# Performance work log

Measured on AMD Instinct MI355X. Metric: run time of the kernel, lower is better.

The kernel has to match this reference:

```python
import jax, jax.numpy as jnp
import numpy as np

H = 512  # hidden_dim

def _gru_dir(x, w_ih, w_hh, b_ih, b_hh, reverse):
    """One direction of one GRU layer. x: [B,T,D]. Returns (outputs [B,T,H], h_T [B,H])."""
    B = x.shape[0]
    # Precompute input-to-gate projections for all timesteps: [T,B,3H]
    xg = (jnp.einsum('btd,gd->btg', x, w_ih) + b_ih).transpose(1, 0, 2)
    if reverse:
        xg = jnp.flip(xg, axis=0)

    def step(h, xg_t):
        hg = h @ w_hh.T + b_hh                      # [B,3H]
        xr, xz, xn = jnp.split(xg_t, 3, axis=-1)
        hr, hz, hn = jnp.split(hg, 3, axis=-1)
        r = jax.nn.sigmoid(xr + hr)
        z = jax.nn.sigmoid(xz + hz)
        n = jnp.tanh(xn + r * hn)
        h_new = (1.0 - z) * n + z * h
        return h_new, h_new

    h0 = jnp.zeros((B, H), dtype=x.dtype)
    hT, hs = jax.lax.scan(step, h0, xg)             # hs: [T,B,H]
    if reverse:
        hs = jnp.flip(hs, axis=0)
    return hs.transpose(1, 0, 2), hT


def _bigru_layer(x, w_ih, w_hh, b_ih, b_hh):
    """Bidirectional layer; stacked weights have leading dim 2 = [fwd, bwd]."""
    out_f, hT_f = _gru_dir(x, w_ih[0], w_hh[0], b_ih[0], b_hh[0], reverse=False)
    out_b, hT_b = _gru_dir(x, w_ih[1], w_hh[1], b_ih[1], b_hh[1], reverse=True)
    return jnp.concatenate([out_f, out_b], axis=-1), hT_f, hT_b


def setup_inputs() -> dict:
    key = jax.random.key(0)
    ks = jax.random.split(key, 12)
    s = 1.0 / np.sqrt(H)
    inp = {
        'sentence': jax.random.randint(ks[0], (64, 512), 0, 50000),
        'emb':      jax.random.normal(ks[1], (50000, 256), jnp.float32) * 0.1,
        'w_ih_l0':  jax.random.normal(ks[2], (2, 3 * H, 256), jnp.float32) * s,
        'w_hh_l0':  jax.random.normal(ks[3], (2, 3 * H, H), jnp.float32) * s,
        'b_ih_l0':  jax.random.normal(ks[4], (2, 3 * H), jnp.float32) * s,
        'b_hh_l0':  jax.random.normal(ks[5], (2, 3 * H), jnp.float32) * s,
        'w_ih_l1':  jax.random.normal(ks[6], (2, 3 * H, 2 * H), jnp.float32) * s,
        'w_hh_l1':  jax.random.normal(ks[7], (2, 3 * H, H), jnp.float32) * s,
        'b_ih_l1':  jax.random.normal(ks[8], (2, 3 * H), jnp.float32) * s,
        'b_hh_l1':  jax.random.normal(ks[9], (2, 3 * H), jnp.float32) * s,
        'fc_w':     jax.random.normal(ks[10], (10, 2 * H), jnp.float32) * s,
        'fc_b':     jax.random.normal(ks[11], (10,), jnp.float32) * s,
    }
    return inp


def reference(sentence, emb, w_ih_l0, w_hh_l0, b_ih_l0, b_hh_l0,
              w_ih_l1, w_hh_l1, b_ih_l1, b_hh_l1, fc_w, fc_b):
    x = emb[sentence]                                # [B,T,E] embedding lookup
    x, _, _ = _bigru_layer(x, w_ih_l0, w_hh_l0, b_ih_l0, b_hh_l0)  # [B,T,2H]
    # dropout is inactive in eval mode
    _, hT_f, hT_b = _bigru_layer(x, w_ih_l1, w_hh_l1, b_ih_l1, b_hh_l1)
    hidden = jnp.concatenate([hT_f, hT_b], axis=1)   # [B,2H] = cat(h[-2], h[-1])
    return hidden @ fc_w.T + fc_b                    # [B,n_classes]
```

## Files before the change

### kernel.cpp

```cpp
#include <hip/hip_runtime.h>
#include <stdint.h>

#define H   512
#define B   64
#define T   512
#define E   256
#define G3  1536
#define CT  64
#define NBG 4
#define NUG 32

typedef short s16;
typedef unsigned short u16;
typedef unsigned int u32;
typedef __attribute__((ext_vector_type(8))) short   short8;
typedef __attribute__((ext_vector_type(4))) float   f32x4;
typedef __attribute__((ext_vector_type(4))) unsigned int u32x4;
typedef __attribute__((ext_vector_type(2))) unsigned int u32x2;
typedef __bf16 bf8_t __attribute__((ext_vector_type(8)));

__device__ __forceinline__ u16 f2b(float f) {
    union { float f; unsigned int i; } v; v.f = f;
    unsigned int r = v.i + 0x7FFF + ((v.i >> 16) & 1);
    return (u16)(r >> 16);
}
__device__ __forceinline__ float sigm(float x)  { return 1.f / (1.f + __expf(-x)); }
__device__ __forceinline__ float tanhs(float x) { return 1.f - 2.f / (1.f + __expf(2.f * x)); }

__global__ void k_cvt(const float* __restrict__ src, u16* __restrict__ dst, int n) {
    int i = blockIdx.x * 256 + threadIdx.x;
    int stride = gridDim.x * 256;
    for (; i < n; i += stride) dst[i] = f2b(src[i]);
}

__global__ void k_init(float* __restrict__ h32, u32* __restrict__ slots) {
    int i = blockIdx.x * 256 + threadIdx.x;
    slots[i] = 0;
    if (i < 65536) h32[i] = 0.f;
}

#define BM 128
#define BN 128
#define BK 32

__global__ __launch_bounds__(256)
void k_gemm_xg(const int* __restrict__ sent, const void* __restrict__ Abuf, int aIsF32,
               const u16* __restrict__ Wbf, const float* __restrict__ bih,
               float* __restrict__ xgT, int K, int c) {
    int d  = blockIdx.z;
    int t0 = d ? (T - (c + 1) * CT) : c * CT;
    const u16* Bw = Wbf + (long)d * G3 * K;
    const float* bias = bih + (long)d * G3;
    float* C = xgT + (long)d * (long)CT * G3 * B;

    __shared__ __align__(16) s16 lA[BM * BK];
    __shared__ __align__(16) s16 lB[BN * BK];

    int tid  = threadIdx.x;
    int lane = tid & 63;
    int wv   = tid >> 6;
    int wm   = wv >> 1, wn = wv & 1;
    int q    = lane >> 4, r16 = lane & 15;

    long m0 = (long)blockIdx.x * BM;
    long n0 = (long)blockIdx.y * BN;

    const float* rowAf[2];
    const s16*   rowAh[2];
    const u16*   rowB[2];
    #pragma unroll
    for (int i = 0; i < 2; i++) {
        int ch = tid + i * 256;
        int r  = ch >> 2, cc = (ch & 3) * 8;
        long m = m0 + r;
        int  bb_ = (int)(m & 63), tl = (int)(m >> 6);
        int  t  = t0 + tl;
        if (aIsF32) rowAf[i] = (const float*)Abuf + (long)sent[bb_ * T + t] * K + cc;
        else        rowAh[i] = (const s16*)Abuf + ((long)bb_ * T + t) * K + cc;
        rowB[i] = Bw + (n0 + r) * K + cc;
    }

    f32x4 acc[4][4];
    #pragma unroll
    for (int i = 0; i < 4; i++)
        #pragma unroll
        for (int j = 0; j < 4; j++) acc[i][j] = (f32x4){0.f, 0.f, 0.f, 0.f};

    for (long k0 = 0; k0 < K; k0 += BK) {
        #pragma unroll
        for (int i = 0; i < 2; i++) {
            if (aIsF32) {
                float4 v0 = *(const float4*)(rowAf[i] + k0);
                float4 v1 = *(const float4*)(rowAf[i] + k0 + 4);
                short8 pk;
                pk[0] = (s16)f2b(v0.x); pk[1] = (s16)f2b(v0.y);
                pk[2] = (s16)f2b(v0.z); pk[3] = (s16)f2b(v0.w);
                pk[4] = (s16)f2b(v1.x); pk[5] = (s16)f2b(v1.y);
                pk[6] = (s16)f2b(v1.z); pk[7] = (s16)f2b(v1.w);
                ((short8*)lA)[tid + i * 256] = pk;
            } else {
                ((short8*)lA)[tid + i * 256] = *(const short8*)(rowAh[i] + k0);
            }
            ((short8*)lB)[tid + i * 256] = *(const short8*)((const s16*)rowB[i] + k0);
        }
        __syncthreads();

        bf8_t af[4], bf[4];
        #pragma unroll
        for (int mt = 0; mt < 4; mt++)
            af[mt] = ((const bf8_t*)lA)[(wm * 64 + mt * 16 + r16) * 4 + q];
        #pragma unroll
        for (int nt = 0; nt < 4; nt++)
            bf[nt] = ((const bf8_t*)lB)[(wn * 64 + nt * 16 + r16) * 4 + q];
        #pragma unroll
        for (int mt = 0; mt < 4; mt++)
            #pragma unroll
            for (int nt = 0; nt < 4; nt++)
                acc[mt][nt] = __builtin_amdgcn_mfma_f32_16x16x32_bf16(
                                  bf[nt], af[mt], acc[mt][nt], 0, 0, 0);
        __syncthreads();
    }

    #pragma unroll
    for (int nt = 0; nt < 4; nt++) {
        f32x4 bv = *(const f32x4*)(bias + n0 + wn * 64 + nt * 16 + q * 4);
        #pragma unroll
        for (int mt = 0; mt < 4; mt++) {
            long m = m0 + wm * 64 + mt * 16 + r16;
            long tl = m >> 6, b = m & 63;
            #pragma unroll
            for (int rg = 0; rg < 4; rg++) {
                long n = n0 + wn * 64 + nt * 16 + q * 4 + rg;
                C[(tl * G3 + n) * B + b] = acc[mt][nt][rg] + bv[rg];
            }
        }
    }
}

__global__ __launch_bounds__(64, 1)
void k_chunk(const u16* __restrict__ Whhbf, const float* __restrict__ bhh,
             const float* __restrict__ xgT, float* __restrict__ h32,
             u32* __restrict__ slots, int c, u16* __restrict__ x1out, int writeX1) {
    int ug = blockIdx.x;
    int bg = blockIdx.y;
    int d  = blockIdx.z;
    int lane = threadIdx.x;
    int q = lane >> 4, cc = lane & 15;
    int u0 = ug * 16;
    int bgl = bg * 16 + cc;

    const u16* W    = Whhbf + (long)d * G3 * H;
    const float* bb = bhh + (long)d * G3;
    const float* xgf = xgT + (long)d * (long)CT * G3 * B;
    float* h32d = h32 + (long)d * B * H;
    char* slotbase = (char*)slots;

    bf8_t w[3][16];
    #pragma unroll
    for (int gate = 0; gate < 3; gate++)
        #pragma unroll
        for (int kc = 0; kc < 16; kc++)
            w[gate][kc] = *(const bf8_t*)(W + (long)(gate * H + u0 + cc) * H + kc * 32 + q * 8);

    f32x4 brv = *(const f32x4*)(bb + u0 + q * 4);
    f32x4 bzv = *(const f32x4*)(bb + H + u0 + q * 4);
    f32x4 bnv = *(const f32x4*)(bb + 2 * H + u0 + q * 4);

    f32x4 hp = *(const f32x4*)(h32d + (long)bgl * H + u0 + q * 4);

    int jw = ug * 4 + q;
    long off_wr = (long)((jw >> 3) * 2 + (jw & 1)) * 1024
                + (long)((jw >> 1) & 3) * 256 + cc * 16;

    int base = c * CT;

    for (int sl = 0; sl < CT; sl++) {
        int s    = base + sl;
        int tl   = d ? (CT - 1 - sl) : sl;
        int time = d ? (T - 1 - s) : s;
        int tgt  = s;
        u32 st1  = (u32)(s + 1);

        const float* xgb = xgf + ((long)tl * G3 + u0 + q * 4) * B + bgl;
        float xr[4], xz[4], xn[4];
        #pragma unroll
        for (int jj = 0; jj < 4; jj++) {
            xr[jj] = xgb[(long)jj * B];
            xz[jj] = xgb[(long)H * B + (long)jj * B];
            xn[jj] = xgb[(long)2 * H * B + (long)jj * B];
        }

        const char* domb = slotbase + (long)(((d * 2 + (s & 1)) * 4 + bg) * 32768);
        const char* pb  = domb + lane * 16;
        const char* qa0 = pb;
        const char* qa1 = pb + 4096;
        const char* qa2 = pb + 8192;
        const char* qa3 = pb + 12288;
        const char* qa4 = pb + 16384;
        const char* qa5 = pb + 20480;
        const char* qa6 = pb + 24576;
        const char* qa7 = pb + 28672;
        u32x4 p0,p1,p2,p3,p4,p5,p6,p7,p8,p9,p10,p11,p12,p13,p14,p15;
        u32x4 p16,p17,p18,p19,p20,p21,p22,p23,p24,p25,p26,p27,p28,p29,p30,p31;

        for (;;) {
            asm volatile(
                "global_load_dwordx4 %0,  %16, off sc0 sc1\n\t"
                "global_load_dwordx4 %1,  %16, off offset:1024 sc0 sc1\n\t"
                "global_load_dwordx4 %2,  %16, off offset:2048 sc0 sc1\n\t"
                "global_load_dwordx4 %3,  %16, off offset:3072 sc0 sc1\n\t"
                "global_load_dwordx4 %4,  %17, off sc0 sc1\n\t"
                "global_load_dwordx4 %5,  %17, off offset:1024 sc0 sc1\n\t"
                "global_load_dwordx4 %6,  %17, off offset:2048 sc0 sc1\n\t"
                "global_load_dwordx4 %7,  %17, off offset:3072 sc0 sc1\n\t"
                "global_load_dwordx4 %8,  %18, off sc0 sc1\n\t"
                "global_load_dwordx4 %9,  %18, off offset:1024 sc0 sc1\n\t"
                "global_load_dwordx4 %10, %18, off offset:2048 sc0 sc1\n\t"
                "global_load_dwordx4 %11, %18, off offset:3072 sc0 sc1\n\t"
                "global_load_dwordx4 %12, %19, off sc0 sc1\n\t"
                "global_load_dwordx4 %13, %19, off offset:1024 sc0 sc1\n\t"
                "global_load_dwordx4 %14, %19, off offset:2048 sc0 sc1\n\t"
                "global_load_dwordx4 %15, %19, off offset:3072 sc0 sc1"
                : "=&v"(p0),"=&v"(p1),"=&v"(p2),"=&v"(p3),
                  "=&v"(p4),"=&v"(p5),"=&v"(p6),"=&v"(p7),
                  "=&v"(p8),"=&v"(p9),"=&v"(p10),"=&v"(p11),
                  "=&v"(p12),"=&v"(p13),"=&v"(p14),"=&v"(p15)
                : "v"(qa0), "v"(qa1), "v"(qa2), "v"(qa3)
                : "memory");
            asm volatile(
                "global_load_dwordx4 %0,  %16, off sc0 sc1\n\t"
                "global_load_dwordx4 %1,  %16, off offset:1024 sc0 sc1\n\t"
                "global_load_dwordx4 %2,  %16, off offset:2048 sc0 sc1\n\t"
                "global_load_dwordx4 %3,  %16, off offset:3072 sc0 sc1\n\t"
                "global_load_dwordx4 %4,  %17, off sc0 sc1\n\t"
                "global_load_dwordx4 %5,  %17, off offset:1024 sc0 sc1\n\t"
                "global_load_dwordx4 %6,  %17, off offset:2048 sc0 sc1\n\t"
                "global_load_dwordx4 %7,  %17, off offset:3072 sc0 sc1\n\t"
                "global_load_dwordx4 %8,  %18, off sc0 sc1\n\t"
                "global_load_dwordx4 %9,  %18, off offset:1024 sc0 sc1\n\t"
                "global_load_dwordx4 %10, %18, off offset:2048 sc0 sc1\n\t"
                "global_load_dwordx4 %11, %18, off offset:3072 sc0 sc1\n\t"
                "global_load_dwordx4 %12, %19, off sc0 sc1\n\t"
                "global_load_dwordx4 %13, %19, off offset:1024 sc0 sc1\n\t"
                "global_load_dwordx4 %14, %19, off offset:2048 sc0 sc1\n\t"
                "global_load_dwordx4 %15, %19, off offset:3072 sc0 sc1\n\t"
                "s_waitcnt vmcnt(0)"
                : "=&v"(p16),"=&v"(p17),"=&v"(p18),"=&v"(p19),
                  "=&v"(p20),"=&v"(p21),"=&v"(p22),"=&v"(p23),
                  "=&v"(p24),"=&v"(p25),"=&v"(p26),"=&v"(p27),
                  "=&v"(p28),"=&v"(p29),"=&v"(p30),"=&v"(p31)
                : "v"(qa4), "v"(qa5), "v"(qa6), "v"(qa7)
                : "memory");
            __builtin_amdgcn_sched_barrier(0);
            int mn = min((int)p0[1], (int)p0[3]);
            #define MN2(x) mn = min(mn, min((int)x[1], (int)x[3]));
            MN2(p1)  MN2(p2)  MN2(p3)  MN2(p4)  MN2(p5)  MN2(p6)  MN2(p7)
            MN2(p8)  MN2(p9)  MN2(p10) MN2(p11) MN2(p12) MN2(p13) MN2(p14) MN2(p15)
            MN2(p16) MN2(p17) MN2(p18) MN2(p19) MN2(p20) MN2(p21) MN2(p22) MN2(p23)
            MN2(p24) MN2(p25) MN2(p26) MN2(p27) MN2(p28) MN2(p29) MN2(p30) MN2(p31)
            #undef MN2
            if (__all(mn >= tgt)) break;
        }

        f32x4 aR = (f32x4){0.f,0.f,0.f,0.f};
        f32x4 aZ = (f32x4){0.f,0.f,0.f,0.f};
        f32x4 aN = (f32x4){0.f,0.f,0.f,0.f};
        #define STEP_KC(kc, A_, B_) { \
            u32x4 fw = (u32x4){A_[0], A_[2], B_[0], B_[2]}; \
            bf8_t hb = __builtin_bit_cast(bf8_t, fw); \
            aR = __builtin_amdgcn_mfma_f32_16x16x32_bf16(w[0][kc], hb, aR, 0, 0, 0); \
            aZ = __builtin_amdgcn_mfma_f32_16x16x32_bf16(w[1][kc], hb, aZ, 0, 0, 0); \
            aN = __builtin_amdgcn_mfma_f32_16x16x32_bf16(w[2][kc], hb, aN, 0, 0, 0); }
        STEP_KC(0,  p0,  p1)  STEP_KC(1,  p2,  p3)  STEP_KC(2,  p4,  p5)  STEP_KC(3,  p6,  p7)
        STEP_KC(4,  p8,  p9)  STEP_KC(5,  p10, p11) STEP_KC(6,  p12, p13) STEP_KC(7,  p14, p15)
        STEP_KC(8,  p16, p17) STEP_KC(9,  p18, p19) STEP_KC(10, p20, p21) STEP_KC(11, p22, p23)
        STEP_KC(12, p24, p25) STEP_KC(13, p26, p27) STEP_KC(14, p28, p29) STEP_KC(15, p30, p31)
        #undef STEP_KC

        float hh[4];
        #pragma unroll
        for (int rg = 0; rg < 4; rg++) {
            float r = sigm(xr[rg] + aR[rg] + brv[rg]);
            float z = sigm(xz[rg] + aZ[rg] + bzv[rg]);
            float n = tanhs(xn[rg] + r * (aN[rg] + bnv[rg]));
            hh[rg] = (1.f - z) * n + z * hp[rg];
        }
        hp = (f32x4){hh[0], hh[1], hh[2], hh[3]};

        u32 w0 = (u32)f2b(hh[0]) | ((u32)f2b(hh[1]) << 16);
        u32 w1 = (u32)f2b(hh[2]) | ((u32)f2b(hh[3]) << 16);
        u32x4 sv = (u32x4){w0, st1, w1, st1};
        char* ps = slotbase + (long)(((d * 2 + ((s + 1) & 1)) * 4 + bg) * 32768) + off_wr;
        asm volatile("global_store_dwordx4 %0, %1, off sc0 sc1"
                     :: "v"(ps), "v"(sv) : "memory");

        if (writeX1) {
            u32x2 xv = (u32x2){w0, w1};
            *(u32x2*)(x1out + ((long)bgl * T + time) * 1024 + d * H + u0 + q * 4) = xv;
        }
    }

    *(f32x4*)(h32d + (long)bgl * H + u0 + q * 4) = hp;
}

__global__ __launch_bounds__(256)
void k_fc(const float* __restrict__ h32, const float* __restrict__ fcw,
          const float* __restrict__ fcb, float* __restrict__ out) {
    int b   = blockIdx.x;
    int tid = threadIdx.x;
    float p[10];
    #pragma unroll
    for (int o = 0; o < 10; o++) p[o] = 0.f;
    for (int k = tid; k < 1024; k += 256) {
        int dd = k >> 9, kk = k & 511;
        float hv = h32[(long)dd * B * H + (long)b * H + kk];
        #pragma unroll
        for (int o = 0; o < 10; o++) p[o] += hv * fcw[o * 1024 + k];
    }
    __shared__ float red[10][256];
    #pragma unroll
    for (int o = 0; o < 10; o++) red[o][tid] = p[o];
    __syncthreads();
    for (int off = 128; off > 0; off >>= 1) {
        if (tid < off)
            #pragma unroll
            for (int o = 0; o < 10; o++) red[o][tid] += red[o][tid + off];
        __syncthreads();
    }
    if (tid < 10) out[b * 10 + tid] = red[tid][0] + fcb[tid];
}

extern "C" void kernel_launch(void* const* d_in, const int* in_sizes, int n_in,
                              void* d_out, int out_size, void* d_ws, size_t ws_size,
                              hipStream_t stream) {
    const int*   sent = (const int*)d_in[0];
    const float* emb  = (const float*)d_in[1];
    const float* wih0 = (const float*)d_in[2];
    const float* whh0 = (const float*)d_in[3];
    const float* bih0 = (const float*)d_in[4];
    const float* bhh0 = (const float*)d_in[5];
    const float* wih1 = (const float*)d_in[6];
    const float* whh1 = (const float*)d_in[7];
    const float* bih1 = (const float*)d_in[8];
    const float* bhh1 = (const float*)d_in[9];
    const float* fcw  = (const float*)d_in[10];
    const float* fcb  = (const float*)d_in[11];
    float* outp = (float*)d_out;

    char*  ws  = (char*)d_ws;
    float* xg  = (float*)(ws);
    u16*   x1  = (u16*)(ws + 50331648L);
    float* h32 = (float*)(ws + 50331648L + 67108864L);
    u32*   slt = (u32*)(ws + 50331648L + 67108864L + 262144L);
    u16*   wbf = (u16*)(ws + 50331648L + 67108864L + 262144L + 524288L);
    u16* wih0b = wbf;
    u16* wih1b = wbf + 786432L;
    u16* whh0b = wbf + 786432L + 3145728L;
    u16* whh1b = whh0b + 1572864L;

    k_cvt<<<512, 256, 0, stream>>>(wih0, wih0b, 786432);
    k_cvt<<<512, 256, 0, stream>>>(wih1, wih1b, 3145728);
    k_cvt<<<512, 256, 0, stream>>>(whh0, whh0b, 1572864);
    k_cvt<<<512, 256, 0, stream>>>(whh1, whh1b, 1572864);

    dim3 gg(32, 12, 2);
    dim3 gc(NUG, NBG, 2);

    k_init<<<512, 256, 0, stream>>>(h32, slt);
    for (int c = 0; c < T / CT; c++) {
        k_gemm_xg<<<gg, 256, 0, stream>>>(sent, emb, 1, wih0b, bih0, xg, E, c);
        k_chunk<<<gc, 64, 0, stream>>>(whh0b, bhh0, xg, h32, slt, c, x1, 1);
    }

    k_init<<<512, 256, 0, stream>>>(h32, slt);
    for (int c = 0; c < T / CT; c++) {
        k_gemm_xg<<<gg, 256, 0, stream>>>(sent, x1, 0, wih1b, bih1, xg, 2 * H, c);
        k_chunk<<<gc, 64, 0, stream>>>(whh1b, bhh1, xg, h32, slt, c, (u16*)nullptr, 0);
    }

    k_fc<<<B, 256, 0, stream>>>(h32, fcw, fcb, outp);
}
```

Before: 3.314 ms.

## Use XCD-local cache scope for slot polling with fallback, remap blocks per domain

```diff
diff --git a/kernel.cpp b/kernel.cpp
--- a/kernel.cpp
+++ b/kernel.cpp
@@ -137,13 +137,64 @@
     }
 }
 
+#define BULK(SC) \
+    asm volatile( \
+        "global_load_dwordx4 %0,  %16, off " SC "\n\t" \
+        "global_load_dwordx4 %1,  %16, off offset:1024 " SC "\n\t" \
+        "global_load_dwordx4 %2,  %16, off offset:2048 " SC "\n\t" \
+        "global_load_dwordx4 %3,  %16, off offset:3072 " SC "\n\t" \
+        "global_load_dwordx4 %4,  %17, off " SC "\n\t" \
+        "global_load_dwordx4 %5,  %17, off offset:1024 " SC "\n\t" \
+        "global_load_dwordx4 %6,  %17, off offset:2048 " SC "\n\t" \
+        "global_load_dwordx4 %7,  %17, off offset:3072 " SC "\n\t" \
+        "global_load_dwordx4 %8,  %18, off " SC "\n\t" \
+        "global_load_dwordx4 %9,  %18, off offset:1024 " SC "\n\t" \
+        "global_load_dwordx4 %10, %18, off offset:2048 " SC "\n\t" \
+        "global_load_dwordx4 %11, %18, off offset:3072 " SC "\n\t" \
+        "global_load_dwordx4 %12, %19, off " SC "\n\t" \
+        "global_load_dwordx4 %13, %19, off offset:1024 " SC "\n\t" \
+        "global_load_dwordx4 %14, %19, off offset:2048 " SC "\n\t" \
+        "global_load_dwordx4 %15, %19, off offset:3072 " SC \
+        : "=&v"(p0),"=&v"(p1),"=&v"(p2),"=&v"(p3), \
+          "=&v"(p4),"=&v"(p5),"=&v"(p6),"=&v"(p7), \
+          "=&v"(p8),"=&v"(p9),"=&v"(p10),"=&v"(p11), \
+          "=&v"(p12),"=&v"(p13),"=&v"(p14),"=&v"(p15) \
+        : "v"(qa0), "v"(qa1), "v"(qa2), "v"(qa3) \
+        : "memory"); \
+    asm volatile( \
+        "global_load_dwordx4 %0,  %16, off " SC "\n\t" \
+        "global_load_dwordx4 %1,  %16, off offset:1024 " SC "\n\t" \
+        "global_load_dwordx4 %2,  %16, off offset:2048 " SC "\n\t" \
+        "global_load_dwordx4 %3,  %16, off offset:3072 " SC "\n\t" \
+        "global_load_dwordx4 %4,  %17, off " SC "\n\t" \
+        "global_load_dwordx4 %5,  %17, off offset:1024 " SC "\n\t" \
+        "global_load_dwordx4 %6,  %17, off offset:2048 " SC "\n\t" \
+        "global_load_dwordx4 %7,  %17, off offset:3072 " SC "\n\t" \
+        "global_load_dwordx4 %8,  %18, off " SC "\n\t" \
+        "global_load_dwordx4 %9,  %18, off offset:1024 " SC "\n\t" \
+        "global_load_dwordx4 %10, %18, off offset:2048 " SC "\n\t" \
+        "global_load_dwordx4 %11, %18, off offset:3072 " SC "\n\t" \
+        "global_load_dwordx4 %12, %19, off " SC "\n\t" \
+        "global_load_dwordx4 %13, %19, off offset:1024 " SC "\n\t" \
+        "global_load_dwordx4 %14, %19, off offset:2048 " SC "\n\t" \
+        "global_load_dwordx4 %15, %19, off offset:3072 " SC "\n\t" \
+        "s_waitcnt vmcnt(0)" \
+        : "=&v"(p16),"=&v"(p17),"=&v"(p18),"=&v"(p19), \
+          "=&v"(p20),"=&v"(p21),"=&v"(p22),"=&v"(p23), \
+          "=&v"(p24),"=&v"(p25),"=&v"(p26),"=&v"(p27), \
+          "=&v"(p28),"=&v"(p29),"=&v"(p30),"=&v"(p31) \
+        : "v"(qa4), "v"(qa5), "v"(qa6), "v"(qa7) \
+        : "memory");
+
 __global__ __launch_bounds__(64, 1)
 void k_chunk(const u16* __restrict__ Whhbf, const float* __restrict__ bhh,
              const float* __restrict__ xgT, float* __restrict__ h32,
              u32* __restrict__ slots, int c, u16* __restrict__ x1out, int writeX1) {
-    int ug = blockIdx.x;
-    int bg = blockIdx.y;
-    int d  = blockIdx.z;
+    int bid = blockIdx.x;
+    int dom = bid & 7;
+    int ug  = bid >> 3;
+    int d   = dom >> 2;
+    int bg  = dom & 3;
     int lane = threadIdx.x;
     int q = lane >> 4, cc = lane & 15;
     int u0 = ug * 16;
@@ -173,6 +224,7 @@
                 + (long)((jw >> 1) & 3) * 256 + cc * 16;
 
     int base = c * CT;
+    bool fast = true;
 
     for (int sl = 0; sl < CT; sl++) {
         int s    = base + sl;
@@ -203,54 +255,10 @@
         u32x4 p0,p1,p2,p3,p4,p5,p6,p7,p8,p9,p10,p11,p12,p13,p14,p15;
         u32x4 p16,p17,p18,p19,p20,p21,p22,p23,p24,p25,p26,p27,p28,p29,p30,p31;
 
+        int fails = 0;
         for (;;) {
-            asm volatile(
-                "global_load_dwordx4 %0,  %16, off sc0 sc1\n\t"
-                "global_load_dwordx4 %1,  %16, off offset:1024 sc0 sc1\n\t"
-                "global_load_dwordx4 %2,  %16, off offset:2048 sc0 sc1\n\t"
-                "global_load_dwordx4 %3,  %16, off offset:3072 sc0 sc1\n\t"
-                "global_load_dwordx4 %4,  %17, off sc0 sc1\n\t"
-                "global_load_dwordx4 %5,  %17, off offset:1024 sc0 sc1\n\t"
-                "global_load_dwordx4 %6,  %17, off offset:2048 sc0 sc1\n\t"
-                "global_load_dwordx4 %7,  %17, off offset:3072 sc0 sc1\n\t"
-                "global_load_dwordx4 %8,  %18, off sc0 sc1\n\t"
-                "global_load_dwordx4 %9,  %18, off offset:1024 sc0 sc1\n\t"
-                "global_load_dwordx4 %10, %18, off offset:2048 sc0 sc1\n\t"
-                "global_load_dwordx4 %11, %18, off offset:3072 sc0 sc1\n\t"
-                "global_load_dwordx4 %12, %19, off sc0 sc1\n\t"
-                "global_load_dwordx4 %13, %19, off offset:1024 sc0 sc1\n\t"
-                "global_load_dwordx4 %14, %19, off offset:2048 sc0 sc1\n\t"
-                "global_load_dwordx4 %15, %19, off offset:3072 sc0 sc1"
-                : "=&v"(p0),"=&v"(p1),"=&v"(p2),"=&v"(p3),
-                  "=&v"(p4),"=&v"(p5),"=&v"(p6),"=&v"(p7),
-                  "=&v"(p8),"=&v"(p9),"=&v"(p10),"=&v"(p11),
-                  "=&v"(p12),"=&v"(p13),"=&v"(p14),"=&v"(p15)
-                : "v"(qa0), "v"(qa1), "v"(qa2), "v"(qa3)
-                : "memory");
-            asm volatile(
-                "global_load_dwordx4 %0,  %16, off sc0 sc1\n\t"
-                "global_load_dwordx4 %1,  %16, off offset:1024 sc0 sc1\n\t"
-                "global_load_dwordx4 %2,  %16, off offset:2048 sc0 sc1\n\t"
-                "global_load_dwordx4 %3,  %16, off offset:3072 sc0 sc1\n\t"
-                "global_load_dwordx4 %4,  %17, off sc0 sc1\n\t"
-                "global_load_dwordx4 %5,  %17, off offset:1024 sc0 sc1\n\t"
-                "global_load_dwordx4 %6,  %17, off offset:2048 sc0 sc1\n\t"
-                "global_load_dwordx4 %7,  %17, off offset:3072 sc0 sc1\n\t"
-                "global_load_dwordx4 %8,  %18, off sc0 sc1\n\t"
-                "global_load_dwordx4 %9,  %18, off offset:1024 sc0 sc1\n\t"
-                "global_load_dwordx4 %10, %18, off offset:2048 sc0 sc1\n\t"
-                "global_load_dwordx4 %11, %18, off offset:3072 sc0 sc1\n\t"
-                "global_load_dwordx4 %12, %19, off sc0 sc1\n\t"
-                "global_load_dwordx4 %13, %19, off offset:1024 sc0 sc1\n\t"
-                "global_load_dwordx4 %14, %19, off offset:2048 sc0 sc1\n\t"
-                "global_load_dwordx4 %15, %19, off offset:3072 sc0 sc1\n\t"
-                "s_waitcnt vmcnt(0)"
-                : "=&v"(p16),"=&v"(p17),"=&v"(p18),"=&v"(p19),
-                  "=&v"(p20),"=&v"(p21),"=&v"(p22),"=&v"(p23),
-                  "=&v"(p24),"=&v"(p25),"=&v"(p26),"=&v"(p27),
-                  "=&v"(p28),"=&v"(p29),"=&v"(p30),"=&v"(p31)
-                : "v"(qa4), "v"(qa5), "v"(qa6), "v"(qa7)
-                : "memory");
+            if (fast) { BULK("sc0") }
+            else      { BULK("sc0 sc1") }
             __builtin_amdgcn_sched_barrier(0);
             int mn = min((int)p0[1], (int)p0[3]);
             #define MN2(x) mn = min(mn, min((int)x[1], (int)x[3]));
@@ -260,6 +268,7 @@
             MN2(p24) MN2(p25) MN2(p26) MN2(p27) MN2(p28) MN2(p29) MN2(p30) MN2(p31)
             #undef MN2
             if (__all(mn >= tgt)) break;
+            if (++fails > 8) fast = false;
         }
 
         f32x4 aR = (f32x4){0.f,0.f,0.f,0.f};
@@ -291,6 +300,8 @@
         u32 w1 = (u32)f2b(hh[2]) | ((u32)f2b(hh[3]) << 16);
         u32x4 sv = (u32x4){w0, st1, w1, st1};
         char* ps = slotbase + (long)(((d * 2 + ((s + 1) & 1)) * 4 + bg) * 32768) + off_wr;
+        asm volatile("global_store_dwordx4 %0, %1, off sc0"
+                     :: "v"(ps), "v"(sv) : "memory");
         asm volatile("global_store_dwordx4 %0, %1, off sc0 sc1"
                      :: "v"(ps), "v"(sv) : "memory");
 
@@ -302,6 +313,7 @@
 
     *(f32x4*)(h32d + (long)bgl * H + u0 + q * 4) = hp;
 }
+#undef BULK
 
 __global__ __launch_bounds__(256)
 void k_fc(const float* __restrict__ h32, const float* __restrict__ fcw,
@@ -364,18 +376,17 @@
     k_cvt<<<512, 256, 0, stream>>>(whh1, whh1b, 1572864);
 
     dim3 gg(32, 12, 2);
-    dim3 gc(NUG, NBG, 2);
 
     k_init<<<512, 256, 0, stream>>>(h32, slt);
     for (int c = 0; c < T / CT; c++) {
         k_gemm_xg<<<gg, 256, 0, stream>>>(sent, emb, 1, wih0b, bih0, xg, E, c);
-        k_chunk<<<gc, 64, 0, stream>>>(whh0b, bhh0, xg, h32, slt, c, x1, 1);
+        k_chunk<<<256, 64, 0, stream>>>(whh0b, bhh0, xg, h32, slt, c, x1, 1);
     }
 
     k_init<<<512, 256, 0, stream>>>(h32, slt);
     for (int c = 0; c < T / CT; c++) {
         k_gemm_xg<<<gg, 256, 0, stream>>>(sent, x1, 0, wih1b, bih1, xg, 2 * H, c);
-        k_chunk<<<gc, 64, 0, stream>>>(whh1b, bhh1, xg, h32, slt, c, (u16*)nullptr, 0);
+        k_chunk<<<256, 64, 0, stream>>>(whh1b, bhh1, xg, h32, slt, c, (u16*)nullptr, 0);
     }
 
     k_fc<<<B, 256, 0, stream>>>(h32, fcw, fcb, outp);
```

New measurement: 3.072 ms. -7.3%, faster.
